# Performance work log

Hardware: AMD Instinct MI355X
Metric: run time of the kernel (lower is better)

Reference implementation:

```python
import jax, jax.numpy as jnp
import numpy as np

DEPTH = 8            # 2**DEPTH - 1 = 255 internal nodes, 2**DEPTH = 256 leaves
BATCH = 2048
NUM_CLASSES = 200
EPS = 1e-07


def setup_inputs() -> dict:
    key = jax.random.key(0)
    k_sim, k_leaf = jax.random.split(key)
    # similarities[i] is the LOG prob of routing right at internal node i
    # (heap order: children of i are 2i+1, 2i+2). Log-probs are <= 0.
    sims = -(jax.random.uniform(k_sim, (2 ** DEPTH - 1, BATCH), dtype=jnp.float32) * 3.0 + 0.01)
    leaf_logits = jax.random.normal(k_leaf, (2 ** DEPTH, NUM_CLASSES), dtype=jnp.float32)
    return {"similarities": sims, "leaf_logits": leaf_logits}


def reference(similarities, leaf_logits):
    B = similarities.shape[1]
    C = leaf_logits.shape[1]
    log2 = jnp.asarray(np.log(2.0), dtype=similarities.dtype)
    # Leaf log-distributions, broadcast over batch: [n_leaves, B, C]
    dists = jnp.broadcast_to(jax.nn.log_softmax(leaf_logits, axis=-1)[:, None, :],
                             (leaf_logits.shape[0], B, C))
    # Bottom-up over tree levels (fixed small loop over DEPTH levels).
    for level in reversed(range(DEPTH)):
        n = 2 ** level
        p_right = similarities[n - 1: 2 * n - 1][:, :, None]   # [n, B, 1]
        a = jnp.abs(p_right) + EPS
        # numerically-stable log(1 - exp(-a)), split at log(2) as in the source
        p_left = jnp.where(a < log2,
                           jnp.log(-jnp.expm1(-a)),
                           jnp.log1p(-jnp.exp(-a)))
        # children of level-l node j are the consecutive pair (2j, 2j+1) in level l+1
        dists = jnp.logaddexp(p_left + dists[0::2], p_right + dists[1::2])  # [n, B, C]
    return dists[0]  # root pred_logits: [B, C]
```

## Files before the change

kernel.cpp:

```cpp
#include <hip/hip_runtime.h>

#define DEPTH 8
#define NINT 255
#define NLEAF 256
#define BATCH 2048
#define NCLS 200
#define EPS 1e-7f
#define TB 8

__global__ __launch_bounds__(64) void leaf_softmax_kernel(
    const float* __restrict__ logits, float* __restrict__ S) {
    const int l = blockIdx.x;
    const int t = threadIdx.x;
    const float* row = logits + l * NCLS;

    float v[4];
    float m = -1e30f;
#pragma unroll
    for (int k = 0; k < 4; ++k) {
        int c = t + 64 * k;
        v[k] = (c < NCLS) ? row[c] : -1e30f;
        m = fmaxf(m, v[k]);
    }
#pragma unroll
    for (int off = 32; off >= 1; off >>= 1)
        m = fmaxf(m, __shfl_xor(m, off, 64));

    float e[4];
    float s = 0.f;
#pragma unroll
    for (int k = 0; k < 4; ++k) {
        e[k] = expf(v[k] - m);
        s += e[k];
    }
#pragma unroll
    for (int off = 32; off >= 1; off >>= 1)
        s += __shfl_xor(s, off, 64);

    const float inv = 1.0f / s;
#pragma unroll
    for (int k = 0; k < 4; ++k) {
        int c = t + 64 * k;
        if (c < NCLS) S[l * NCLS + c] = e[k] * inv;
    }
}

__global__ __launch_bounds__(256) void tree_gemm_fused(
    const float* __restrict__ sims, const float* __restrict__ S,
    float* __restrict__ out) {
    __shared__ float pr_s[NINT * TB];
    __shared__ float pl_s[NINT * TB];
    __shared__ float W[NLEAF * TB];

    const int tid = threadIdx.x;
    const int b0 = blockIdx.x * TB;

    for (int idx = tid; idx < NINT * TB; idx += 256) {
        const int node = idx >> 3;
        const int b = idx & (TB - 1);
        const float pr = sims[node * BATCH + b0 + b];
        const float a = EPS - pr;
        const float pl = (a < 0.6931472f) ? logf(-expm1f(-a))
                                          : log1pf(-expf(-a));
        pr_s[idx] = pr;
        pl_s[idx] = pl;
    }
    __syncthreads();

    for (int idx = tid; idx < NLEAF * TB; idx += 256) {
        const int l = idx >> 3;
        const int b = idx & (TB - 1);
        float w = 0.f;
        int n = NINT + l;
#pragma unroll
        for (int d = 0; d < DEPTH; ++d) {
            const int p = (n - 1) >> 1;
            const bool right = ((n & 1) == 0);
            w += right ? pr_s[p * TB + b] : pl_s[p * TB + b];
            n = p;
        }
        W[idx] = expf(w);
    }
    __syncthreads();

    const int tc = tid & 63;
    const int tb = tid >> 6;
    const int c0 = tc * 4;
    const int bb = tb * 2;
    if (c0 < NCLS) {
        float acc[2][4] = {};
#pragma unroll 16
        for (int l = 0; l < NLEAF; ++l) {
            const float4 s4 = *reinterpret_cast<const float4*>(S + l * NCLS + c0);
            const float2 w2 = *reinterpret_cast<const float2*>(&W[l * TB + bb]);
            const float sv[4] = {s4.x, s4.y, s4.z, s4.w};
            const float wv[2] = {w2.x, w2.y};
#pragma unroll
            for (int i = 0; i < 2; ++i)
#pragma unroll
                for (int j = 0; j < 4; ++j)
                    acc[i][j] += wv[i] * sv[j];
        }
#pragma unroll
        for (int i = 0; i < 2; ++i) {
            float4 o;
            o.x = logf(acc[i][0]);
            o.y = logf(acc[i][1]);
            o.z = logf(acc[i][2]);
            o.w = logf(acc[i][3]);
            *reinterpret_cast<float4*>(out + (size_t)(b0 + bb + i) * NCLS + c0) = o;
        }
    }
}

extern "C" void kernel_launch(void* const* d_in, const int* in_sizes, int n_in,
                              void* d_out, int out_size, void* d_ws, size_t ws_size,
                              hipStream_t stream) {
    const float* sims = (const float*)d_in[0];
    const float* logits = (const float*)d_in[1];
    float* S = (float*)d_ws;
    float* out = (float*)d_out;

    leaf_softmax_kernel<<<NLEAF, 64, 0, stream>>>(logits, S);
    tree_gemm_fused<<<BATCH / TB, 256, 0, stream>>>(sims, S, out);
}
```

Baseline: 76.40 us.

## Fuse leaf softmax into tree kernel and compute leaf mixing with bf16 MFMA

Drops the separate leaf-softmax launch. Each block now recomputes exp of the leaf logits into shared memory as bf16, transposed, and folds the softmax normaliser into the path weights. The leaf-weight by class contraction runs on 16x16x32 bf16 MFMA instructions instead of scalar FMAs, and the sims loads are issued before the exp work to overlap latency. This removes a launch and the scalar GEMM cost, but adds redundant per-block exp work over all 256x200 logits and lowers the accumulation inputs to bf16 precision.

```diff
diff --git a/kernel.cpp b/kernel.cpp
--- a/kernel.cpp
+++ b/kernel.cpp
@@ -7,108 +7,133 @@
 #define NCLS 200
 #define EPS 1e-7f
 #define TB 8
+#define LPAD 264
+#define NTILE 13
 
-__global__ __launch_bounds__(64) void leaf_softmax_kernel(
-    const float* __restrict__ logits, float* __restrict__ S) {
-    const int l = blockIdx.x;
-    const int t = threadIdx.x;
-    const float* row = logits + l * NCLS;
+typedef float f32x4 __attribute__((ext_vector_type(4)));
+typedef __bf16 bf16x8 __attribute__((ext_vector_type(8)));
 
-    float v[4];
-    float m = -1e30f;
-#pragma unroll
-    for (int k = 0; k < 4; ++k) {
-        int c = t + 64 * k;
-        v[k] = (c < NCLS) ? row[c] : -1e30f;
-        m = fmaxf(m, v[k]);
-    }
-#pragma unroll
-    for (int off = 32; off >= 1; off >>= 1)
-        m = fmaxf(m, __shfl_xor(m, off, 64));
-
-    float e[4];
-    float s = 0.f;
-#pragma unroll
-    for (int k = 0; k < 4; ++k) {
-        e[k] = expf(v[k] - m);
-        s += e[k];
-    }
-#pragma unroll
-    for (int off = 32; off >= 1; off >>= 1)
-        s += __shfl_xor(s, off, 64);
-
-    const float inv = 1.0f / s;
-#pragma unroll
-    for (int k = 0; k < 4; ++k) {
-        int c = t + 64 * k;
-        if (c < NCLS) S[l * NCLS + c] = e[k] * inv;
-    }
+static __device__ __forceinline__ unsigned short f2bf(float f) {
+    unsigned int u = __builtin_bit_cast(unsigned int, f);
+    u += 0x7fffu + ((u >> 16) & 1u);
+    return (unsigned short)(u >> 16);
 }
 
-__global__ __launch_bounds__(256) void tree_gemm_fused(
-    const float* __restrict__ sims, const float* __restrict__ S,
+__global__ __launch_bounds__(256) void tree_fused(
+    const float* __restrict__ sims, const float* __restrict__ logits,
     float* __restrict__ out) {
+    __shared__ unsigned short Et[(NTILE * 16) * LPAD];
+    __shared__ unsigned short Wt[16 * LPAD];
     __shared__ float pr_s[NINT * TB];
     __shared__ float pl_s[NINT * TB];
-    __shared__ float W[NLEAF * TB];
+    __shared__ float invZ[NLEAF];
 
     const int tid = threadIdx.x;
     const int b0 = blockIdx.x * TB;
 
-    for (int idx = tid; idx < NINT * TB; idx += 256) {
-        const int node = idx >> 3;
-        const int b = idx & (TB - 1);
-        const float pr = sims[node * BATCH + b0 + b];
-        const float a = EPS - pr;
-        const float pl = (a < 0.6931472f) ? logf(-expm1f(-a))
-                                          : log1pf(-expf(-a));
-        pr_s[idx] = pr;
-        pl_s[idx] = pl;
+    float prv[8];
+#pragma unroll
+    for (int p = 0; p < 8; ++p) {
+        const int idx = tid + 256 * p;
+        if (idx < NINT * TB)
+            prv[p] = sims[(idx >> 3) * BATCH + b0 + (idx & 7)];
+    }
+
+    {
+        unsigned int* wz = (unsigned int*)(Wt + 8 * LPAD);
+        unsigned int* ez = (unsigned int*)(Et + 200 * LPAD);
+        for (int i = tid; i < (8 * LPAD) / 2; i += 256) { wz[i] = 0u; ez[i] = 0u; }
+    }
+
+    {
+        const float4* lr = (const float4*)(logits + tid * NCLS);
+        float Z = 0.f;
+        for (int j = 0; j < NCLS / 4; ++j) {
+            const float4 v = lr[j];
+            const float e0 = __expf(v.x), e1 = __expf(v.y),
+                        e2 = __expf(v.z), e3 = __expf(v.w);
+            Z += (e0 + e1) + (e2 + e3);
+            const int c = 4 * j;
+            Et[(c + 0) * LPAD + tid] = f2bf(e0);
+            Et[(c + 1) * LPAD + tid] = f2bf(e1);
+            Et[(c + 2) * LPAD + tid] = f2bf(e2);
+            Et[(c + 3) * LPAD + tid] = f2bf(e3);
+        }
+        invZ[tid] = 1.0f / Z;
+    }
+
+#pragma unroll
+    for (int p = 0; p < 8; ++p) {
+        const int idx = tid + 256 * p;
+        if (idx < NINT * TB) {
+            const float pr = prv[p];
+            const float a = EPS - pr;
+            const float pl = (a < 0.6931472f) ? logf(-expm1f(-a))
+                                              : log1pf(-expf(-a));
+            pr_s[idx] = pr;
+            pl_s[idx] = pl;
+        }
     }
     __syncthreads();
 
-    for (int idx = tid; idx < NLEAF * TB; idx += 256) {
+#pragma unroll
+    for (int p = 0; p < 8; ++p) {
+        const int idx = tid + 256 * p;
         const int l = idx >> 3;
-        const int b = idx & (TB - 1);
+        const int b = idx & 7;
         float w = 0.f;
         int n = NINT + l;
 #pragma unroll
         for (int d = 0; d < DEPTH; ++d) {
-            const int p = (n - 1) >> 1;
-            const bool right = ((n & 1) == 0);
-            w += right ? pr_s[p * TB + b] : pl_s[p * TB + b];
-            n = p;
+            const int par = (n - 1) >> 1;
+            w += ((n & 1) == 0) ? pr_s[par * TB + b] : pl_s[par * TB + b];
+            n = par;
         }
-        W[idx] = expf(w);
+        Wt[b * LPAD + l] = f2bf(__expf(w) * invZ[l]);
     }
     __syncthreads();
 
-    const int tc = tid & 63;
-    const int tb = tid >> 6;
-    const int c0 = tc * 4;
-    const int bb = tb * 2;
-    if (c0 < NCLS) {
-        float acc[2][4] = {};
-#pragma unroll 16
-        for (int l = 0; l < NLEAF; ++l) {
-            const float4 s4 = *reinterpret_cast<const float4*>(S + l * NCLS + c0);
-            const float2 w2 = *reinterpret_cast<const float2*>(&W[l * TB + bb]);
-            const float sv[4] = {s4.x, s4.y, s4.z, s4.w};
-            const float wv[2] = {w2.x, w2.y};
+    const int lane = tid & 63;
+    const int wave = tid >> 6;
+    const int mn = lane & 15;
+    const int quad = lane >> 4;
+
+    f32x4 acc0 = {0.f, 0.f, 0.f, 0.f};
+    f32x4 acc1 = {0.f, 0.f, 0.f, 0.f};
+    f32x4 acc2 = {0.f, 0.f, 0.f, 0.f};
+    f32x4 acc3 = {0.f, 0.f, 0.f, 0.f};
+    const int t0 = wave, t1 = wave + 4, t2 = wave + 8, t3 = wave + 12;
+
 #pragma unroll
-            for (int i = 0; i < 2; ++i)
+    for (int s = 0; s < 8; ++s) {
+        const int ko = s * 32 + quad * 8;
+        const bf16x8 a = *(const bf16x8*)(Wt + mn * LPAD + ko);
+        const bf16x8 bv0 = *(const bf16x8*)(Et + (t0 * 16 + mn) * LPAD + ko);
+        acc0 = __builtin_amdgcn_mfma_f32_16x16x32_bf16(a, bv0, acc0, 0, 0, 0);
+        const bf16x8 bv1 = *(const bf16x8*)(Et + (t1 * 16 + mn) * LPAD + ko);
+        acc1 = __builtin_amdgcn_mfma_f32_16x16x32_bf16(a, bv1, acc1, 0, 0, 0);
+        const bf16x8 bv2 = *(const bf16x8*)(Et + (t2 * 16 + mn) * LPAD + ko);
+        acc2 = __builtin_amdgcn_mfma_f32_16x16x32_bf16(a, bv2, acc2, 0, 0, 0);
+        if (wave == 0) {
+            const bf16x8 bv3 = *(const bf16x8*)(Et + (t3 * 16 + mn) * LPAD + ko);
+            acc3 = __builtin_amdgcn_mfma_f32_16x16x32_bf16(a, bv3, acc3, 0, 0, 0);
+        }
+    }
+
+    if (quad < 2) {
+        const int rbase = b0 + quad * 4;
 #pragma unroll
-                for (int j = 0; j < 4; ++j)
-                    acc[i][j] += wv[i] * sv[j];
-        }
+        for (int i = 0; i < 4; ++i) {
+            const int t = (i == 0) ? t0 : (i == 1) ? t1 : (i == 2) ? t2 : t3;
+            if (t >= NTILE) continue;
+            const f32x4 acc = (i == 0) ? acc0 : (i == 1) ? acc1
+                            : (i == 2) ? acc2 : acc3;
+            const int c = t * 16 + mn;
+            if (c < NCLS) {
 #pragma unroll
-        for (int i = 0; i < 2; ++i) {
-            float4 o;
-            o.x = logf(acc[i][0]);
-            o.y = logf(acc[i][1]);
-            o.z = logf(acc[i][2]);
-            o.w = logf(acc[i][3]);
-            *reinterpret_cast<float4*>(out + (size_t)(b0 + bb + i) * NCLS + c0) = o;
+                for (int r = 0; r < 4; ++r)
+                    out[(size_t)(rbase + r) * NCLS + c] = __logf(acc[r]);
+            }
         }
     }
 }
@@ -118,9 +143,6 @@
                               hipStream_t stream) {
     const float* sims = (const float*)d_in[0];
     const float* logits = (const float*)d_in[1];
-    float* S = (float*)d_ws;
     float* out = (float*)d_out;
-
-    leaf_softmax_kernel<<<NLEAF, 64, 0, stream>>>(logits, S);
-    tree_gemm_fused<<<BATCH / TB, 256, 0, stream>>>(sims, S, out);
+    tree_fused<<<BATCH / TB, 256, 0, stream>>>(sims, logits, out);
 }
```

After: 73.58 us. 3.7% less time.
